# Performance work log

Hardware: AMD Instinct MI355X
Metric: run time of the kernel (lower is better)

The kernel has to match this reference:

```python
import jax, jax.numpy as jnp
import numpy as np

DIM = 1024
NH = 16
HD = DIM // NH  # 64
WINDOW = 8      # window_size; flash window=(WINDOW-1, -1) with causal=True
EPS_NORM = 1e-6


def _rmsnorm(h, w):
    # RMSNorm over last dim (full model dim, applied before head split)
    return h * jax.lax.rsqrt(jnp.mean(h * h, axis=-1, keepdims=True) + EPS_NORM) * w


def _rope(h, cos, sin):
    # h: [bv, L, NH, HD]; cos/sin: [L, HD//2]; torch view-as-complex pairs adjacent elems
    hr = h[..., 0::2]
    hi = h[..., 1::2]
    c = cos[None, :, None, :]
    s = sin[None, :, None, :]
    out_r = hr * c - hi * s
    out_i = hr * s + hi * c
    return jnp.stack([out_r, out_i], axis=-1).reshape(h.shape)


def setup_inputs() -> dict:
    key = jax.random.key(0)
    ks = jax.random.split(key, 8)
    bv, f, nlt = 1, 16, 1472
    b = bv * f
    L = f * nlt
    wscale = DIM ** -0.5
    x = jax.random.normal(ks[0], (b, nlt, DIM), jnp.float32)
    # standard RoPE tables, base 10000, d//2 frequencies
    pos = jnp.arange(L, dtype=jnp.float32)[:, None]
    inv_freq = 1.0 / (10000.0 ** (jnp.arange(HD // 2, dtype=jnp.float32) / (HD // 2)))
    ang = pos * inv_freq[None, :]
    inp = {
        'x': x,
        'freqs_cos': jnp.cos(ang),
        'freqs_sin': jnp.sin(ang),
        'q_w': jax.random.normal(ks[1], (DIM, DIM), jnp.float32) * wscale,
        'q_b': jnp.zeros((DIM,), jnp.float32),
        'k_w': jax.random.normal(ks[2], (DIM, DIM), jnp.float32) * wscale,
        'k_b': jnp.zeros((DIM,), jnp.float32),
        'v_w': jax.random.normal(ks[3], (DIM, DIM), jnp.float32) * wscale,
        'v_b': jnp.zeros((DIM,), jnp.float32),
        'o_w': jax.random.normal(ks[4], (DIM, DIM), jnp.float32) * wscale,
        'o_b': jnp.zeros((DIM,), jnp.float32),
        'norm_q_w': jnp.ones((DIM,), jnp.float32),
        'norm_k_w': jnp.ones((DIM,), jnp.float32),
        'bv': 1,
        'f': 16,
        'nlt': 1472,
    }
    return inp


def reference(x, freqs_cos, freqs_sin, q_w, q_b, k_w, k_b, v_w, v_b, o_w, o_b,
              norm_q_w, norm_k_w, bv, f, nlt):
    b, s = x.shape[:2]  # b = bv*f, s = nlt
    q = _rmsnorm(x @ q_w.T + q_b, norm_q_w)
    k = _rmsnorm(x @ k_w.T + k_b, norm_k_w)
    v = (x @ v_w.T + v_b).reshape(bv, f, s, NH, HD)
    # RoPE over flattened (frame, token) positions
    q4 = q.reshape(bv, f * s, NH, HD)
    k4 = k.reshape(bv, f * s, NH, HD)
    qr = _rope(q4, freqs_cos, freqs_sin)
    kr = _rope(k4, freqs_cos, freqs_sin)
    # temporal layout: [bv*nlt, f, NH, HD] (attend over frames per latent token)
    qr = qr.reshape(bv, f, s, NH, HD).transpose(0, 2, 1, 3, 4).reshape(bv * s, f, NH, HD)
    kr = kr.reshape(bv, f, s, NH, HD).transpose(0, 2, 1, 3, 4).reshape(bv * s, f, NH, HD)
    vr = v.transpose(0, 2, 1, 3, 4).reshape(bv * s, f, NH, HD)
    # causal sliding-window mask over frames: j <= i and i - j < WINDOW
    fi = jnp.arange(f)
    mask = (fi[None, :] <= fi[:, None]) & (fi[:, None] - fi[None, :] < WINDOW)  # [f, f]
    scores = jnp.einsum('bqhd,bkhd->bhqk', qr, kr) / np.float32(np.sqrt(HD))
    scores = jnp.where(mask[None, None], scores, jnp.float32(-1e30))
    attn = jax.nn.softmax(scores, axis=-1)
    o = jnp.einsum('bhqk,bkhd->bqhd', attn, vr)  # [bv*nlt, f, NH, HD]
    o = o.reshape(bv, s, f, NH, HD).transpose(0, 2, 1, 3, 4).reshape(bv * f, s, DIM)
    return o @ o_w.T + o_b
```

## Files before the change

kernel.cpp:

```cpp
#include <hip/hip_runtime.h>
#include <hip/hip_bf16.h>
#include <math.h>

typedef __bf16 bf16;
typedef bf16 bf16x8 __attribute__((ext_vector_type(8)));
typedef bf16 bf16x4 __attribute__((ext_vector_type(4)));
typedef float f32x4 __attribute__((ext_vector_type(4)));

#define NFRM 16
#define SEQ  1472
#define TOK  (NFRM * SEQ)
#define DIM_ 1024
#define NH_  16
#define HD_  64
#define KROW 1032


__device__ __forceinline__ void load_lds_16B(const void* g, void* l) {
  __builtin_amdgcn_global_load_lds(
      (const __attribute__((address_space(1))) unsigned int*)g,
      (__attribute__((address_space(3))) unsigned int*)l,
      16, 0, 0);
}

__global__ __launch_bounds__(256) void cvt_bf16(const float* __restrict__ s,
                                                bf16* __restrict__ d, int n) {
  size_t i = ((size_t)blockIdx.x * 256 + threadIdx.x) * 8;
  if (i >= (size_t)n) return;
  const int r   = (int)(i >> 10);
  const int col = (int)(i & 1023);
  const int f   = r / SEQ;
  const int t   = r - f * SEQ;
  const size_t o = ((size_t)(t * 16 + f) << 10) + col;
  f32x4 a = *(const f32x4*)(s + i);
  f32x4 b = *(const f32x4*)(s + i + 4);
  bf16x8 v;
  v[0] = (bf16)a[0]; v[1] = (bf16)a[1]; v[2] = (bf16)a[2]; v[3] = (bf16)a[3];
  v[4] = (bf16)b[0]; v[5] = (bf16)b[1]; v[6] = (bf16)b[2]; v[7] = (bf16)b[3];
  *(bf16x8*)(d + o) = v;
}

__global__ __launch_bounds__(256) void cvt_w4(
    const float* __restrict__ w0, const float* __restrict__ w1,
    const float* __restrict__ w2, const float* __restrict__ w3,
    bf16* __restrict__ d0, bf16* __restrict__ d1,
    bf16* __restrict__ d2, bf16* __restrict__ d3) {
  const int z = blockIdx.y;
  const float* s = (z == 0) ? w0 : (z == 1) ? w1 : (z == 2) ? w2 : w3;
  bf16* d       = (z == 0) ? d0 : (z == 1) ? d1 : (z == 2) ? d2 : d3;
  size_t i = ((size_t)blockIdx.x * 256 + threadIdx.x) * 8;
  f32x4 a = *(const f32x4*)(s + i);
  f32x4 b = *(const f32x4*)(s + i + 4);
  bf16x8 o;
  o[0] = (bf16)a[0]; o[1] = (bf16)a[1]; o[2] = (bf16)a[2]; o[3] = (bf16)a[3];
  o[4] = (bf16)b[0]; o[5] = (bf16)b[1]; o[6] = (bf16)b[2]; o[7] = (bf16)b[3];
  *(bf16x8*)(d + i) = o;
}

__device__ __forceinline__ void swz368(int h, int& bx, int& by) {
  const int s = (h & 7) * 46 + (h >> 3);
  bx = s >> 2;
  by = s & 3;
}

template <typename OutT, int OMAP>
__device__ __forceinline__ void gemm256_body(const bf16* __restrict__ A,
                                             const bf16* __restrict__ B,
                                             const float* __restrict__ bias,
                                             OutT* __restrict__ C,
                                             bf16* lds, int bx, int by) {
  const int tid  = threadIdx.x;
  const int w    = tid >> 6;
  const int lane = tid & 63;
  const int am0  = bx * 256;
  const int bn0  = by * 256;

  const int rstep = w * 8 + (lane >> 3);
  const int jsrc  = ((lane & 7) ^ ((lane >> 3) & 7)) * 8;
  const int arb[4] = {0, 128, 64, 192};
  const bf16* srcp[8];
  int dstoff[8];
#pragma unroll
  for (int s = 0; s < 4; ++s) {
    srcp[s]   = B + (size_t)(bn0 + s * 64 + rstep) * DIM_ + jsrc;
    dstoff[s] = 32768 + s * 8192 + w * 1024;
    srcp[4 + s]   = A + (size_t)(am0 + arb[s] + rstep) * DIM_ + jsrc;
    dstoff[4 + s] = arb[s] * 128 + w * 1024;
  }

  const int wr   = w >> 2;
  const int wc   = w & 3;
  const int frow = lane & 15;
  const int g    = lane >> 4;
  const int sw   = (frow & 7) << 4;
  const int e0   = (g * 16) ^ sw;
  const int e1   = (g * 16 + 64) ^ sw;
  const int aA   = (wr * 128 + frow) * 128;
  const int bB   = 32768 + (wc * 64 + frow) * 128;

  f32x4 acc[8][4];
#pragma unroll
  for (int i = 0; i < 8; ++i)
#pragma unroll
    for (int j = 0; j < 4; ++j) {
      f32x4 z = {0.f, 0.f, 0.f, 0.f};
      acc[i][j] = z;
    }

  char* ldsc = (char*)lds;

#pragma unroll
  for (int s = 0; s < 8; ++s) load_lds_16B(srcp[s], ldsc + dstoff[s]);

#pragma unroll 1
  for (int it = 0; it < 8; ++it) {
#pragma unroll
    for (int half = 0; half < 2; ++half) {
      const int kt   = it * 2 + half;
      const int cur  = half ? 65536 : 0;
      const int nxt  = half ? 0 : 65536;
      const int kpre = (kt < 15) ? (kt + 1) * 64 : 15 * 64;

      asm volatile("s_waitcnt vmcnt(2)" ::: "memory");
      asm volatile("s_barrier" ::: "memory");
#pragma unroll
      for (int s = 0; s < 4; ++s)
        load_lds_16B(srcp[s] + kpre, ldsc + nxt + dstoff[s]);

      bf16x8 bfv[4][2];
#pragma unroll
      for (int j = 0; j < 4; ++j) {
        bfv[j][0] = *(const bf16x8*)(ldsc + cur + bB + j * 2048 + e0);
        bfv[j][1] = *(const bf16x8*)(ldsc + cur + bB + j * 2048 + e1);
      }

#pragma unroll
      for (int p = 0; p < 4; ++p) {
        if (p == 1) {
          load_lds_16B(srcp[4] + kpre, ldsc + nxt + dstoff[4]);
          load_lds_16B(srcp[5] + kpre, ldsc + nxt + dstoff[5]);
        }
        if (p == 2) {
          asm volatile("s_waitcnt vmcnt(6)" ::: "memory");
          asm volatile("s_barrier" ::: "memory");
          load_lds_16B(srcp[6] + kpre, ldsc + nxt + dstoff[6]);
          load_lds_16B(srcp[7] + kpre, ldsc + nxt + dstoff[7]);
        }
        bf16x8 af[2][2];
#pragma unroll
        for (int ii = 0; ii < 2; ++ii) {
          const int i = p * 2 + ii;
          af[ii][0] = *(const bf16x8*)(ldsc + cur + aA + i * 2048 + e0);
          af[ii][1] = *(const bf16x8*)(ldsc + cur + aA + i * 2048 + e1);
        }
        __builtin_amdgcn_s_setprio(1);
#pragma unroll
        for (int ii = 0; ii < 2; ++ii) {
          const int i = p * 2 + ii;
#pragma unroll
          for (int j = 0; j < 4; ++j) {
            acc[i][j] = __builtin_amdgcn_mfma_f32_16x16x32_bf16(
                af[ii][0], bfv[j][0], acc[i][j], 0, 0, 0);
            acc[i][j] = __builtin_amdgcn_mfma_f32_16x16x32_bf16(
                af[ii][1], bfv[j][1], acc[i][j], 0, 0, 0);
          }
        }
        __builtin_amdgcn_s_setprio(0);
      }
    }
  }

  const int cl = lane & 15;
  const int rq = g * 4;
#pragma unroll
  for (int j = 0; j < 4; ++j) {
    const int nc   = bn0 + wc * 64 + j * 16 + cl;
    const float bb = bias[nc];
#pragma unroll
    for (int i = 0; i < 8; ++i) {
#pragma unroll
      for (int r = 0; r < 4; ++r) {
        const int rowp = am0 + wr * 128 + i * 16 + rq + r;
        const size_t mr = (OMAP == 1)
            ? ((size_t)(rowp & 15) * SEQ + (rowp >> 4))
            : (size_t)rowp;
        C[mr * DIM_ + nc] = (OutT)(acc[i][j][r] + bb);
      }
    }
  }
}

__global__ __launch_bounds__(512, 2) void gemm_qkv(
    const bf16* __restrict__ A,
    const bf16* __restrict__ Bq, const bf16* __restrict__ Bk,
    const bf16* __restrict__ Bv,
    const float* __restrict__ bq, const float* __restrict__ bk,
    const float* __restrict__ bv,
    bf16* __restrict__ Cq, bf16* __restrict__ Ck, bf16* __restrict__ Cv) {
  __shared__ __align__(16) bf16 lds[65536];
  const int z = blockIdx.z;
  const bf16* B    = (z == 0) ? Bq : (z == 1) ? Bk : Bv;
  const float* bia = (z == 0) ? bq : (z == 1) ? bk : bv;
  bf16* C          = (z == 0) ? Cq : (z == 1) ? Ck : Cv;
  int bx, by;
  swz368(blockIdx.y * 92 + blockIdx.x, bx, by);
  gemm256_body<bf16, 0>(A, B, bia, C, lds, bx, by);
}

__global__ __launch_bounds__(512, 2) void gemm_out(
    const bf16* __restrict__ A, const bf16* __restrict__ B,
    const float* __restrict__ bias, float* __restrict__ C) {
  __shared__ __align__(16) bf16 lds[65536];
  int bx, by;
  swz368(blockIdx.y * 92 + blockIdx.x, bx, by);
  gemm256_body<float, 1>(A, B, bias, C, lds, bx, by);
}

__global__ __launch_bounds__(256) void norm_rope(
    bf16* __restrict__ q, bf16* __restrict__ k,
    const float* __restrict__ nqw, const float* __restrict__ nkw,
    const float* __restrict__ fcos, const float* __restrict__ fsin) {
  const int lane = threadIdx.x & 63, wave = threadIdx.x >> 6;
  const size_t row  = (size_t)blockIdx.x * 4 + wave;
  const size_t base = row * DIM_;
  const size_t pos  = (row & 15) * (size_t)SEQ + (row >> 4);
  const int e0 = lane * 16;
  const int j0 = (lane & 3) * 8;

  float cs[8], sn[8];
#pragma unroll
  for (int i = 0; i < 8; ++i) {
    cs[i] = fcos[pos * 32 + j0 + i];
    sn[i] = fsin[pos * 32 + j0 + i];
  }

  bf16x8 qa = *(const bf16x8*)(q + base + e0);
  bf16x8 qb = *(const bf16x8*)(q + base + e0 + 8);
  bf16x8 ka = *(const bf16x8*)(k + base + e0);
  bf16x8 kb = *(const bf16x8*)(k + base + e0 + 8);

  float xq[16], xk[16];
#pragma unroll
  for (int i = 0; i < 8; ++i) {
    xq[i] = (float)qa[i]; xq[8 + i] = (float)qb[i];
    xk[i] = (float)ka[i]; xk[8 + i] = (float)kb[i];
  }
  float sq = 0.f, sk = 0.f;
#pragma unroll
  for (int i = 0; i < 16; ++i) { sq += xq[i] * xq[i]; sk += xk[i] * xk[i]; }
#pragma unroll
  for (int off = 32; off > 0; off >>= 1) {
    sq += __shfl_xor(sq, off);
    sk += __shfl_xor(sk, off);
  }
  const float rq = rsqrtf(sq * (1.0f / 1024.0f) + 1e-6f);
  const float rk = rsqrtf(sk * (1.0f / 1024.0f) + 1e-6f);
#pragma unroll
  for (int i = 0; i < 16; ++i) {
    xq[i] *= rq * nqw[e0 + i];
    xk[i] *= rk * nkw[e0 + i];
  }
  bf16x8 oa, ob, oc, od;
#pragma unroll
  for (int p = 0; p < 8; ++p) {
    const float c = cs[p], s = sn[p];
    const float q0 = xq[2 * p], q1 = xq[2 * p + 1];
    const float k0 = xk[2 * p], k1 = xk[2 * p + 1];
    const float qr = q0 * c - q1 * s, qi = q0 * s + q1 * c;
    const float kr = k0 * c - k1 * s, ki = k0 * s + k1 * c;
    if (p < 4) { oa[2 * p] = (bf16)qr; oa[2 * p + 1] = (bf16)qi;
                 oc[2 * p] = (bf16)kr; oc[2 * p + 1] = (bf16)ki; }
    else       { ob[2 * p - 8] = (bf16)qr; ob[2 * p - 7] = (bf16)qi;
                 od[2 * p - 8] = (bf16)kr; od[2 * p - 7] = (bf16)ki; }
  }
  *(bf16x8*)(q + base + e0)     = oa;
  *(bf16x8*)(q + base + e0 + 8) = ob;
  *(bf16x8*)(k + base + e0)     = oc;
  *(bf16x8*)(k + base + e0 + 8) = od;
}

__global__ __launch_bounds__(512, 4) void attn_win(
    const bf16* __restrict__ q, const bf16* __restrict__ k,
    const bf16* __restrict__ v, bf16* __restrict__ o) {
  __shared__ __align__(16) bf16 ks[16 * KROW];
  __shared__ __align__(16) bf16 vs[16 * KROW];
  __shared__ __align__(16) bf16 ps[16 * 256];
  const int t    = blockIdx.x;
  const int tid  = threadIdx.x;
  const int wave = tid >> 6, lane = tid & 63;
  const size_t tb = (size_t)t * (16 * DIM_);

#pragma unroll
  for (int i = 0; i < 4; ++i) {
    const int j = wave * 4 + i;
    const int r = j >> 1, half = j & 1;
    const size_t g = tb + (size_t)r * DIM_ + half * 512 + lane * 8;
    load_lds_16B(k + g, ks + r * KROW + half * 512);
    load_lds_16B(v + g, vs + r * KROW + half * 512);
  }
  __syncthreads();

  const int fl  = lane & 15;
  const int kq  = (lane >> 4) * 8;
#pragma unroll
  for (int hh = 0; hh < 2; ++hh) {
    const int h = wave * 2 + hh;
    const size_t qg = tb + (size_t)fl * DIM_ + h * HD_ + kq;
    bf16x8 aq0 = *(const bf16x8*)(q + qg);
    bf16x8 aq1 = *(const bf16x8*)(q + qg + 32);
    const int ko = fl * KROW + h * HD_ + kq;
    bf16x8 bk0 = *(const bf16x8*)(ks + ko);
    bf16x8 bk1 = *(const bf16x8*)(ks + ko + 32);
    f32x4 sc = {0.f, 0.f, 0.f, 0.f};
    sc = __builtin_amdgcn_mfma_f32_16x16x32_bf16(aq0, bk0, sc, 0, 0, 0);
    sc = __builtin_amdgcn_mfma_f32_16x16x32_bf16(aq1, bk1, sc, 0, 0, 0);
#pragma unroll
    for (int r = 0; r < 4; ++r) {
      const int row = (lane >> 4) * 4 + r;
      const bool valid = (fl <= row) && (row - fl < 8);
      float s = valid ? sc[r] * 0.125f : -1e30f;
      float m = s;
#pragma unroll
      for (int off = 8; off > 0; off >>= 1) m = fmaxf(m, __shfl_xor(m, off));
      const float e = __expf(s - m);
      float su = e;
#pragma unroll
      for (int off = 8; off > 0; off >>= 1) su += __shfl_xor(su, off);
      ps[h * 256 + row * 16 + fl] = (bf16)(e / su);
    }
  }
  __syncthreads();

  const int h3 = tid >> 5;
  const int dc = (tid >> 2) & 7;
  const int fg = tid & 3;
  bf16x8 pr[8];
#pragma unroll
  for (int i = 0; i < 4; ++i) {
    pr[2 * i]     = *(const bf16x8*)(ps + h3 * 256 + (fg * 4 + i) * 16);
    pr[2 * i + 1] = *(const bf16x8*)(ps + h3 * 256 + (fg * 4 + i) * 16 + 8);
  }
  float acc[4][8];
#pragma unroll
  for (int i = 0; i < 4; ++i)
#pragma unroll
    for (int d = 0; d < 8; ++d) acc[i][d] = 0.f;

  const bf16* vb = vs + h3 * HD_ + dc * 8;
#pragma unroll
  for (int fk2 = 0; fk2 < 16; ++fk2) {
    bf16x8 vv8 = *(const bf16x8*)(vb + fk2 * KROW);
    float vf[8];
#pragma unroll
    for (int d = 0; d < 8; ++d) vf[d] = (float)vv8[d];
#pragma unroll
    for (int i = 0; i < 4; ++i) {
      const float pp = (float)((fk2 < 8) ? pr[2 * i][fk2] : pr[2 * i + 1][fk2 - 8]);
#pragma unroll
      for (int d = 0; d < 8; ++d) acc[i][d] += pp * vf[d];
    }
  }
#pragma unroll
  for (int i = 0; i < 4; ++i) {
    bf16x8 ov;
#pragma unroll
    for (int d = 0; d < 8; ++d) ov[d] = (bf16)acc[i][d];
    *(bf16x8*)(o + tb + (size_t)(fg * 4 + i) * DIM_ + h3 * HD_ + dc * 8) = ov;
  }
}

extern "C" void kernel_launch(void* const* d_in, const int* in_sizes, int n_in,
                              void* d_out, int out_size, void* d_ws,
                              size_t ws_size, hipStream_t stream) {
  const float* x    = (const float*)d_in[0];
  const float* fcos = (const float*)d_in[1];
  const float* fsin = (const float*)d_in[2];
  const float* q_w  = (const float*)d_in[3];
  const float* q_b  = (const float*)d_in[4];
  const float* k_w  = (const float*)d_in[5];
  const float* k_b  = (const float*)d_in[6];
  const float* v_w  = (const float*)d_in[7];
  const float* v_b  = (const float*)d_in[8];
  const float* o_w  = (const float*)d_in[9];
  const float* o_b  = (const float*)d_in[10];
  const float* nqw  = (const float*)d_in[11];
  const float* nkw  = (const float*)d_in[12];
  float* out = (float*)d_out;

  char* ws = (char*)d_ws;
  const size_t SZ  = (size_t)TOK * DIM_ * 2;
  const size_t WSZ = (size_t)DIM_ * DIM_ * 2;
  bf16* xb = (bf16*)(ws);
  bf16* wq = (bf16*)(ws + SZ);
  bf16* wk = (bf16*)(ws + SZ + WSZ);
  bf16* wv = (bf16*)(ws + SZ + 2 * WSZ);
  bf16* wo = (bf16*)(ws + SZ + 3 * WSZ);
  bf16* qq = (bf16*)(ws + SZ + 4 * WSZ);
  bf16* kk = (bf16*)(ws + SZ + 4 * WSZ + SZ);
  bf16* vv = (bf16*)(ws + SZ + 4 * WSZ + 2 * SZ);
  bf16* om = xb;

  const int NTOT = TOK * DIM_;
  const int NW   = DIM_ * DIM_;

  cvt_bf16<<<NTOT / 2048, 256, 0, stream>>>(x, xb, NTOT);
  cvt_w4<<<dim3(NW / 2048, 4), 256, 0, stream>>>(q_w, k_w, v_w, o_w,
                                                 wq, wk, wv, wo);

  dim3 gq(TOK / 256, DIM_ / 256, 3);
  gemm_qkv<<<gq, 512, 0, stream>>>(xb, wq, wk, wv, q_b, k_b, v_b, qq, kk, vv);

  norm_rope<<<TOK / 4, 256, 0, stream>>>(qq, kk, nqw, nkw, fcos, fsin);

  attn_win<<<SEQ, 512, 0, stream>>>(qq, kk, vv, om);

  gemm_out<<<dim3(TOK / 256, DIM_ / 256), 512, 0, stream>>>(om, wo, o_b, out);
}
```

Before: 536.5 us.

## Fuse RMSNorm and RoPE into windowed attention kernel, reuse LDS for V

Removes the separate norm_rope kernel. Q and K are now loaded into LDS inside attn_win, normalized and rotated in place, and then consumed by the MFMA score step. V is held in registers and written into the reused Q buffer after scoring. This saves one kernel launch and a full read and write pass over q and k in HBM. In exchange it adds an extra barrier and more registers per thread, and the LDS footprint stays the same.

After: 505.3 us. 5.8% less time.

```diff
diff --git a/kernel.cpp b/kernel.cpp
--- a/kernel.cpp
+++ b/kernel.cpp
@@ -216,87 +216,80 @@
   gemm256_body<float, 1>(A, B, bias, C, lds, bx, by);
 }
 
-__global__ __launch_bounds__(256) void norm_rope(
-    bf16* __restrict__ q, bf16* __restrict__ k,
+__global__ __launch_bounds__(512, 4) void attn_win(
+    const bf16* __restrict__ q, const bf16* __restrict__ k,
+    const bf16* __restrict__ v, bf16* __restrict__ o,
     const float* __restrict__ nqw, const float* __restrict__ nkw,
     const float* __restrict__ fcos, const float* __restrict__ fsin) {
-  const int lane = threadIdx.x & 63, wave = threadIdx.x >> 6;
-  const size_t row  = (size_t)blockIdx.x * 4 + wave;
-  const size_t base = row * DIM_;
-  const size_t pos  = (row & 15) * (size_t)SEQ + (row >> 4);
-  const int e0 = lane * 16;
-  const int j0 = (lane & 3) * 8;
-
-  float cs[8], sn[8];
-#pragma unroll
-  for (int i = 0; i < 8; ++i) {
-    cs[i] = fcos[pos * 32 + j0 + i];
-    sn[i] = fsin[pos * 32 + j0 + i];
-  }
-
-  bf16x8 qa = *(const bf16x8*)(q + base + e0);
-  bf16x8 qb = *(const bf16x8*)(q + base + e0 + 8);
-  bf16x8 ka = *(const bf16x8*)(k + base + e0);
-  bf16x8 kb = *(const bf16x8*)(k + base + e0 + 8);
-
-  float xq[16], xk[16];
-#pragma unroll
-  for (int i = 0; i < 8; ++i) {
-    xq[i] = (float)qa[i]; xq[8 + i] = (float)qb[i];
-    xk[i] = (float)ka[i]; xk[8 + i] = (float)kb[i];
-  }
-  float sq = 0.f, sk = 0.f;
-#pragma unroll
-  for (int i = 0; i < 16; ++i) { sq += xq[i] * xq[i]; sk += xk[i] * xk[i]; }
-#pragma unroll
-  for (int off = 32; off > 0; off >>= 1) {
-    sq += __shfl_xor(sq, off);
-    sk += __shfl_xor(sk, off);
-  }
-  const float rq = rsqrtf(sq * (1.0f / 1024.0f) + 1e-6f);
-  const float rk = rsqrtf(sk * (1.0f / 1024.0f) + 1e-6f);
-#pragma unroll
-  for (int i = 0; i < 16; ++i) {
-    xq[i] *= rq * nqw[e0 + i];
-    xk[i] *= rk * nkw[e0 + i];
-  }
-  bf16x8 oa, ob, oc, od;
-#pragma unroll
-  for (int p = 0; p < 8; ++p) {
-    const float c = cs[p], s = sn[p];
-    const float q0 = xq[2 * p], q1 = xq[2 * p + 1];
-    const float k0 = xk[2 * p], k1 = xk[2 * p + 1];
-    const float qr = q0 * c - q1 * s, qi = q0 * s + q1 * c;
-    const float kr = k0 * c - k1 * s, ki = k0 * s + k1 * c;
-    if (p < 4) { oa[2 * p] = (bf16)qr; oa[2 * p + 1] = (bf16)qi;
-                 oc[2 * p] = (bf16)kr; oc[2 * p + 1] = (bf16)ki; }
-    else       { ob[2 * p - 8] = (bf16)qr; ob[2 * p - 7] = (bf16)qi;
-                 od[2 * p - 8] = (bf16)kr; od[2 * p - 7] = (bf16)ki; }
-  }
-  *(bf16x8*)(q + base + e0)     = oa;
-  *(bf16x8*)(q + base + e0 + 8) = ob;
-  *(bf16x8*)(k + base + e0)     = oc;
-  *(bf16x8*)(k + base + e0 + 8) = od;
-}
-
-__global__ __launch_bounds__(512, 4) void attn_win(
-    const bf16* __restrict__ q, const bf16* __restrict__ k,
-    const bf16* __restrict__ v, bf16* __restrict__ o) {
   __shared__ __align__(16) bf16 ks[16 * KROW];
-  __shared__ __align__(16) bf16 vs[16 * KROW];
+  __shared__ __align__(16) bf16 xs[16 * KROW];
   __shared__ __align__(16) bf16 ps[16 * 256];
   const int t    = blockIdx.x;
   const int tid  = threadIdx.x;
   const int wave = tid >> 6, lane = tid & 63;
   const size_t tb = (size_t)t * (16 * DIM_);
 
+  const bf16* vg = v + tb + (size_t)tid * 32;
+  bf16x8 vr0 = *(const bf16x8*)(vg);
+  bf16x8 vr1 = *(const bf16x8*)(vg + 8);
+  bf16x8 vr2 = *(const bf16x8*)(vg + 16);
+  bf16x8 vr3 = *(const bf16x8*)(vg + 24);
+
 #pragma unroll
   for (int i = 0; i < 4; ++i) {
     const int j = wave * 4 + i;
     const int r = j >> 1, half = j & 1;
     const size_t g = tb + (size_t)r * DIM_ + half * 512 + lane * 8;
     load_lds_16B(k + g, ks + r * KROW + half * 512);
-    load_lds_16B(v + g, vs + r * KROW + half * 512);
+    load_lds_16B(q + g, xs + r * KROW + half * 512);
+  }
+  __syncthreads();
+
+#pragma unroll
+  for (int i = 0; i < 4; ++i) {
+    const int m  = wave * 4 + i;
+    const int fr = m & 15;
+    bf16* rowp = ((m < 16) ? xs : ks) + fr * KROW;
+    const float* nw = (m < 16) ? nqw : nkw;
+    bf16x8 a = *(const bf16x8*)(rowp + lane * 8);
+    bf16x8 b = *(const bf16x8*)(rowp + 512 + lane * 8);
+    float xa[8], xb[8];
+    float ssq = 0.f;
+#pragma unroll
+    for (int e = 0; e < 8; ++e) {
+      xa[e] = (float)a[e]; xb[e] = (float)b[e];
+      ssq += xa[e] * xa[e] + xb[e] * xb[e];
+    }
+#pragma unroll
+    for (int off = 32; off > 0; off >>= 1) ssq += __shfl_xor(ssq, off);
+    const float rs = rsqrtf(ssq * (1.0f / 1024.0f) + 1e-6f);
+    float wA[8], wB[8];
+    f32x4 w0 = *(const f32x4*)(nw + lane * 8);
+    f32x4 w1 = *(const f32x4*)(nw + lane * 8 + 4);
+    f32x4 w2 = *(const f32x4*)(nw + 512 + lane * 8);
+    f32x4 w3 = *(const f32x4*)(nw + 512 + lane * 8 + 4);
+#pragma unroll
+    for (int e = 0; e < 4; ++e) {
+      wA[e] = w0[e]; wA[4 + e] = w1[e];
+      wB[e] = w2[e]; wB[4 + e] = w3[e];
+    }
+    const size_t pos = (size_t)fr * SEQ + t;
+    f32x4 cc = *(const f32x4*)(fcos + pos * 32 + (lane & 7) * 4);
+    f32x4 sn = *(const f32x4*)(fsin + pos * 32 + (lane & 7) * 4);
+    bf16x8 oa, ob;
+#pragma unroll
+    for (int p = 0; p < 4; ++p) {
+      const float a0 = xa[2 * p] * rs * wA[2 * p];
+      const float a1 = xa[2 * p + 1] * rs * wA[2 * p + 1];
+      const float b0 = xb[2 * p] * rs * wB[2 * p];
+      const float b1 = xb[2 * p + 1] * rs * wB[2 * p + 1];
+      oa[2 * p]     = (bf16)(a0 * cc[p] - a1 * sn[p]);
+      oa[2 * p + 1] = (bf16)(a0 * sn[p] + a1 * cc[p]);
+      ob[2 * p]     = (bf16)(b0 * cc[p] - b1 * sn[p]);
+      ob[2 * p + 1] = (bf16)(b0 * sn[p] + b1 * cc[p]);
+    }
+    *(bf16x8*)(rowp + lane * 8)       = oa;
+    *(bf16x8*)(rowp + 512 + lane * 8) = ob;
   }
   __syncthreads();
 
@@ -305,12 +298,11 @@
 #pragma unroll
   for (int hh = 0; hh < 2; ++hh) {
     const int h = wave * 2 + hh;
-    const size_t qg = tb + (size_t)fl * DIM_ + h * HD_ + kq;
-    bf16x8 aq0 = *(const bf16x8*)(q + qg);
-    bf16x8 aq1 = *(const bf16x8*)(q + qg + 32);
-    const int ko = fl * KROW + h * HD_ + kq;
-    bf16x8 bk0 = *(const bf16x8*)(ks + ko);
-    bf16x8 bk1 = *(const bf16x8*)(ks + ko + 32);
+    const int qo = fl * KROW + h * HD_ + kq;
+    bf16x8 aq0 = *(const bf16x8*)(xs + qo);
+    bf16x8 aq1 = *(const bf16x8*)(xs + qo + 32);
+    bf16x8 bk0 = *(const bf16x8*)(ks + qo);
+    bf16x8 bk1 = *(const bf16x8*)(ks + qo + 32);
     f32x4 sc = {0.f, 0.f, 0.f, 0.f};
     sc = __builtin_amdgcn_mfma_f32_16x16x32_bf16(aq0, bk0, sc, 0, 0, 0);
     sc = __builtin_amdgcn_mfma_f32_16x16x32_bf16(aq1, bk1, sc, 0, 0, 0);
@@ -331,6 +323,15 @@
   }
   __syncthreads();
 
+  {
+    bf16* vd = xs + (tid >> 5) * KROW + (tid & 31) * 32;
+    *(bf16x8*)(vd)      = vr0;
+    *(bf16x8*)(vd + 8)  = vr1;
+    *(bf16x8*)(vd + 16) = vr2;
+    *(bf16x8*)(vd + 24) = vr3;
+  }
+  __syncthreads();
+
   const int h3 = tid >> 5;
   const int dc = (tid >> 2) & 7;
   const int fg = tid & 3;
@@ -346,7 +347,7 @@
 #pragma unroll
     for (int d = 0; d < 8; ++d) acc[i][d] = 0.f;
 
-  const bf16* vb = vs + h3 * HD_ + dc * 8;
+  const bf16* vb = xs + h3 * HD_ + dc * 8;
 #pragma unroll
   for (int fk2 = 0; fk2 < 16; ++fk2) {
     bf16x8 vv8 = *(const bf16x8*)(vb + fk2 * KROW);
@@ -410,9 +411,7 @@
   dim3 gq(TOK / 256, DIM_ / 256, 3);
   gemm_qkv<<<gq, 512, 0, stream>>>(xb, wq, wk, wv, q_b, k_b, v_b, qq, kk, vv);
 
-  norm_rope<<<TOK / 4, 256, 0, stream>>>(qq, kk, nqw, nkw, fcos, fsin);
-
-  attn_win<<<SEQ, 512, 0, stream>>>(qq, kk, vv, om);
+  attn_win<<<SEQ, 512, 0, stream>>>(qq, kk, vv, om, nqw, nkw, fcos, fsin);
 
   gemm_out<<<dim3(TOK / 256, DIM_ / 256), 512, 0, stream>>>(om, wo, o_b, out);
 }
```
